# Optimization experiments

Measured on AMD Instinct MI355X. Metric: run time of the kernel, lower is better.

The kernel has to match this reference:

```python
import jax, jax.numpy as jnp
import numpy as np

B, T, SEG = 64, 16, 50          # batch, n segments, segment length (cap 50 in original)
E, D, H, F = 512, 512, 8, 2048  # dim_embeddings, dim_encoder, n_heads, dim_ff
DH = D // H
SCALE = float(1.0 / np.sqrt(DH))


def _ln(x, g, b):
    m = jnp.mean(x, -1, keepdims=True)
    v = jnp.var(x, -1, keepdims=True)
    return (x - m) * jax.lax.rsqrt(v + 1e-5) * g + b


def _mha(q_in, kv_in, Wq, Wk, Wv, Wo, kv_lens):
    b, sq, _ = q_in.shape
    sk = kv_in.shape[1]
    q = (q_in @ Wq).reshape(b, sq, H, DH)
    k = (kv_in @ Wk).reshape(b, sk, H, DH)
    v = (kv_in @ Wv).reshape(b, sk, H, DH)
    scores = jnp.einsum('bqhd,bkhd->bhqk', q, k) * SCALE
    mask = jnp.arange(sk)[None, :] < kv_lens[:, None]  # [b, sk] key-padding mask
    scores = jnp.where(mask[:, None, None, :], scores, -1e9)
    a = jax.nn.softmax(scores, axis=-1)
    o = jnp.einsum('bhqk,bkhd->bqhd', a, v).reshape(b, sq, D)
    return o @ Wo


def _ffn(x, W1, W2):
    return jax.nn.relu(x @ W1) @ W2


def _encoder(x, lens, p):
    # TransformerEncoder: project E->D, masked self-attn + FFN, post-LN residuals
    h = x @ p['eWin']
    h = _ln(h + _mha(h, h, p['eWq'], p['eWk'], p['eWv'], p['eWo'], lens), p['eG1'], p['eB1'])
    return _ln(h + _ffn(h, p['eF1'], p['eF2']), p['eG2'], p['eB2'])


def _connection(prev, curr, prev_lens, p):
    # Connection: curr cross-attends over prev (masked by prev_lens) + FFN
    h = _ln(curr + _mha(curr, prev, p['cWq'], p['cWk'], p['cWv'], p['cWo'], prev_lens), p['cG1'], p['cB1'])
    return _ln(h + _ffn(h, p['cF1'], p['cF2']), p['cG2'], p['cB2'])


def _forward(seqs, ends, p):
    first_lens = jnp.minimum(ends[:, 0], SEG)
    encoded = _encoder(seqs[:, :SEG], first_lens, p)  # [B, SEG, D]
    # regular segmentation: ends[b,t] = (t+1)*SEG, so every step uses a full segment
    segs = seqs.reshape(B, T, SEG, E).transpose(1, 0, 2, 3)[1:]        # [T-1, B, SEG, E]
    seg_lens = jnp.minimum(ends[:, 1:] - ends[:, :-1], SEG).T          # [T-1, B]
    prev_lens = jnp.full((B,), SEG, jnp.int32)

    def step(enc, xs):
        seg, lens = xs
        currs = _encoder(seg, lens, p)
        out = _connection(enc, currs, prev_lens, p)
        return out, None  # out[-SEG:] == out since seq_len = min(diff, 50) = SEG

    encoded, _ = jax.lax.scan(step, encoded, (segs, seg_lens))
    return encoded


def setup_inputs():
    key = jax.random.key(0)
    ks = jax.random.split(key, 16)
    g = lambda k, s: jax.random.normal(k, s, jnp.float32) * 0.02
    inp = {
        'seqs': jax.random.normal(ks[0], (B, T * SEG, E), jnp.float32),
        'ends': jnp.broadcast_to((jnp.arange(1, T + 1) * SEG).astype(jnp.int32), (B, T)),
        'eWin': g(ks[1], (E, D)),
        'eWq': g(ks[2], (D, D)), 'eWk': g(ks[3], (D, D)),
        'eWv': g(ks[4], (D, D)), 'eWo': g(ks[5], (D, D)),
        'eG1': jnp.ones(D), 'eB1': jnp.zeros(D),
        'eF1': g(ks[6], (D, F)), 'eF2': g(ks[7], (F, D)),
        'eG2': jnp.ones(D), 'eB2': jnp.zeros(D),
        'cWq': g(ks[8], (D, D)), 'cWk': g(ks[9], (D, D)),
        'cWv': g(ks[10], (D, D)), 'cWo': g(ks[11], (D, D)),
        'cG1': jnp.ones(D), 'cB1': jnp.zeros(D),
        'cF1': g(ks[12], (D, F)), 'cF2': g(ks[13], (F, D)),
        'cG2': jnp.ones(D), 'cB2': jnp.zeros(D),
    }
    return inp


def reference(seqs, ends, eWin, eWq, eWk, eWv, eWo, eG1, eB1, eF1, eF2, eG2, eB2,
              cWq, cWk, cWv, cWo, cG1, cB1, cF1, cF2, cG2, cB2):
    p = dict(eWin=eWin, eWq=eWq, eWk=eWk, eWv=eWv, eWo=eWo, eG1=eG1, eB1=eB1,
             eF1=eF1, eF2=eF2, eG2=eG2, eB2=eB2, cWq=cWq, cWk=cWk, cWv=cWv,
             cWo=cWo, cG1=cG1, cB1=cB1, cF1=cF1, cF2=cF2, cG2=cG2, cB2=cB2)
    return _forward(seqs, ends, p)
```

## Files before the change

kernel.cpp:

```cpp
#include <hip/hip_runtime.h>


#define NB   64
#define NT   16
#define SEGL 50
#define DMODEL 512
#define DFF  2048
#define NHEAD 8
#define DHEAD 64

typedef unsigned short ushort_t;
typedef __attribute__((ext_vector_type(8))) short bfrag;
typedef __attribute__((ext_vector_type(4))) float ffrag;

__device__ __forceinline__ ushort_t f2b(float x) {
    union { float f; unsigned u; } c; c.f = x;
    unsigned r = c.u + 0x7fffu + ((c.u >> 16) & 1u);
    return (ushort_t)(r >> 16);
}

#define GLOAD_LDS16(g, l) __builtin_amdgcn_global_load_lds( \
    (const __attribute__((address_space(1))) void*)(g),      \
    (__attribute__((address_space(3))) void*)(l), 16, 0, 0)

template<int BM, int BN, int WROWS, int WCOLS>
__global__ __launch_bounds__(256) void mfma_gemm(
    const ushort_t* __restrict__ A, int agrp, long long astride,
    const ushort_t* __restrict__ Bt, ushort_t* __restrict__ C,
    int M, int N, int K, int relu)
{
    constexpr int WM = BM / WROWS, WN = BN / WCOLS;
    constexpr int SM = WM / 16, SN = WN / 16;
    constexpr int NSUBA = BM / 16, NSUBB = BN / 16;
    constexpr int NSUB = NSUBA + NSUBB;
    constexpr int NINST = NSUB * 2;
    constexpr int IPW = NINST / 4;
    constexpr int BUFS = NSUB * 1024;
    constexpr int EST = WN + 8;
    constexpr int LDS_KLOOP = 2 * BUFS;
    constexpr int LDS_EPI   = 4 * WM * EST;
    constexpr int LDS_SZ = LDS_KLOOP > LDS_EPI ? LDS_KLOOP : LDS_EPI;
    __shared__ ushort_t lds[LDS_SZ];

    const int tid = threadIdx.x;
    const int wave = tid >> 6, lane = tid & 63;
    const int wrow = wave / WCOLS, wcol = wave % WCOLS;
    const int bm = blockIdx.y * BM, bn = blockIdx.x * BN;
    const int lm = lane & 15, lq = lane >> 4;

    ffrag acc[SM][SN];
#pragma unroll
    for (int i = 0; i < SM; ++i)
#pragma unroll
        for (int j = 0; j < SN; ++j) acc[i][j] = (ffrag){0.f, 0.f, 0.f, 0.f};

    const ushort_t* gptr[IPW];
    int loff[IPW];
#pragma unroll
    for (int e = 0; e < IPW; ++e) {
        int g = wave * IPW + e;
        int s = g >> 1, h = g & 1;
        if (s < NSUBA) {
            int m = bm + s * 16 + lm;
            gptr[e] = A + (long long)(m / agrp) * astride
                        + (long long)(m % agrp) * K + h * 32 + lq * 8;
        } else {
            int n = bn + (s - NSUBA) * 16 + lm;
            gptr[e] = Bt + (long long)n * K + h * 32 + lq * 8;
        }
        loff[e] = s * 1024 + h * 512;
    }

#pragma unroll
    for (int e = 0; e < IPW; ++e)
        GLOAD_LDS16(gptr[e], &lds[loff[e]]);

    const int nk = K >> 6;
    for (int kk = 0; kk < nk; ++kk) {
        __syncthreads();
        if (kk + 1 < nk) {
            const int koff = (kk + 1) << 6;
            const int nb = (kk + 1) & 1;
#pragma unroll
            for (int e = 0; e < IPW; ++e)
                GLOAD_LDS16(gptr[e] + koff, &lds[nb * BUFS + loff[e]]);
        }
        const ushort_t* lb = &lds[(kk & 1) * BUFS];
#pragma unroll
        for (int h = 0; h < 2; ++h) {
            bfrag af[SM], bfg[SN];
#pragma unroll
            for (int i = 0; i < SM; ++i)
                af[i] = *(const bfrag*)&lb[(wrow * SM + i) * 1024 + h * 512 + lane * 8];
#pragma unroll
            for (int j = 0; j < SN; ++j)
                bfg[j] = *(const bfrag*)&lb[(NSUBA + wcol * SN + j) * 1024 + h * 512 + lane * 8];
#pragma unroll
            for (int i = 0; i < SM; ++i)
#pragma unroll
                for (int j = 0; j < SN; ++j)
                    acc[i][j] = __builtin_amdgcn_mfma_f32_16x16x32_bf16(
                        af[i], bfg[j], acc[i][j], 0, 0, 0);
        }
    }

    __syncthreads();
    ushort_t* ep = &lds[wave * WM * EST];
#pragma unroll
    for (int i = 0; i < SM; ++i)
#pragma unroll
        for (int j = 0; j < SN; ++j)
#pragma unroll
            for (int r = 0; r < 4; ++r) {
                int row = i * 16 + lq * 4 + r;
                int col = j * 16 + lm;
                float v = acc[i][j][r];
                if (relu) v = fmaxf(v, 0.f);
                ep[row * EST + col] = f2b(v);
            }
    constexpr int CPR = WN / 8;
    constexpr int RPI = 64 / CPR;
    const int lrow = lane / CPR, lcol = (lane % CPR) * 8;
#pragma unroll
    for (int it = 0; it < WM / RPI; ++it) {
        int row = it * RPI + lrow;
        uint4 v = *(const uint4*)&ep[row * EST + lcol];
        long long grow = bm + wrow * WM + row;
        int gcol = bn + wcol * WN + lcol;
        *(uint4*)&C[grow * N + gcol] = v;
    }
}

__global__ __launch_bounds__(256) void wtrans_k(
    const float* __restrict__ W, ushort_t* __restrict__ Wt, int K, int N)
{
    __shared__ float t[32][33];
    const int bk = blockIdx.y * 32, bn = blockIdx.x * 32;
    const int tx = threadIdx.x & 31, ty = threadIdx.x >> 5;
    for (int i = ty; i < 32; i += 8)
        t[i][tx] = W[(long long)(bk + i) * N + bn + tx];
    __syncthreads();
    for (int i = ty; i < 32; i += 8)
        Wt[(long long)(bn + i) * K + bk + tx] = f2b(t[tx][i]);
}

__global__ __launch_bounds__(256) void cvt_k(
    const float* __restrict__ in, ushort_t* __restrict__ out, long long n)
{
    long long i = ((long long)blockIdx.x * 256 + threadIdx.x) * 8;
    if (i >= n) return;
    float4 a = *(const float4*)(in + i);
    float4 b = *(const float4*)(in + i + 4);
    ushort_t o[8] = {f2b(a.x), f2b(a.y), f2b(a.z), f2b(a.w),
                     f2b(b.x), f2b(b.y), f2b(b.z), f2b(b.w)};
    *(uint4*)(out + i) = *(const uint4*)o;
}

__global__ __launch_bounds__(256) void attn_mfma_k(
    const ushort_t* __restrict__ Q, long long qns, long long qrs,
    const ushort_t* __restrict__ K, const ushort_t* __restrict__ V,
    long long kns, long long kvrs,
    ushort_t* __restrict__ O,
    const int* __restrict__ lens, int G, int t0)
{
    __shared__ ushort_t qs[64][72];
    __shared__ ushort_t ks[64][72];
    __shared__ ushort_t vt[64][72];
    const int n = blockIdx.x >> 3, h = blockIdx.x & 7;
    const int tid = threadIdx.x;
    const int wave = tid >> 6, lane = tid & 63;
    const int lm = lane & 15, lq = lane >> 4;
    int len = SEGL;
    if (lens) {
        int b = n / G, t = t0 + (n % G);
        len = lens[b * NT + t];
        if (len > SEGL) len = SEGL;
    }
    {
        uint4 z = {0, 0, 0, 0};
        uint4* vz = (uint4*)&vt[0][0];
        for (int i = tid; i < 64 * 72 / 8; i += 256) vz[i] = z;
    }
    __syncthreads();
    for (int idx = tid; idx < SEGL * 8; idx += 256) {
        int s = idx >> 3, d8 = (idx & 7) << 3;
        const ushort_t* qp = Q + (long long)n * qns + (long long)s * qrs + h * DHEAD + d8;
        const ushort_t* kp = K + (long long)n * kns + (long long)s * kvrs + h * DHEAD + d8;
        const ushort_t* vp = V + (long long)n * kns + (long long)s * kvrs + h * DHEAD + d8;
        *(uint4*)&qs[s][d8] = *(const uint4*)qp;
        *(uint4*)&ks[s][d8] = *(const uint4*)kp;
        uint4 v4 = *(const uint4*)vp;
        const ushort_t* vv = (const ushort_t*)&v4;
#pragma unroll
        for (int u = 0; u < 8; ++u) vt[d8 + u][s] = vv[u];
    }
    __syncthreads();

    ffrag sc[4];
#pragma unroll
    for (int nt = 0; nt < 4; ++nt) sc[nt] = (ffrag){0.f, 0.f, 0.f, 0.f};
#pragma unroll
    for (int kt = 0; kt < 2; ++kt) {
        bfrag a = *(const bfrag*)&qs[wave * 16 + lm][kt * 32 + lq * 8];
#pragma unroll
        for (int nt = 0; nt < 4; ++nt) {
            bfrag b = *(const bfrag*)&ks[nt * 16 + lm][kt * 32 + lq * 8];
            sc[nt] = __builtin_amdgcn_mfma_f32_16x16x32_bf16(a, b, sc[nt], 0, 0, 0);
        }
    }
    __syncthreads();

#pragma unroll
    for (int r = 0; r < 4; ++r) {
        float x[4];
        float mx = -1e30f;
#pragma unroll
        for (int nt = 0; nt < 4; ++nt) {
            int col = nt * 16 + lm;
            x[nt] = (col < len) ? sc[nt][r] * 0.125f : -1e9f;
            mx = fmaxf(mx, x[nt]);
        }
        for (int off = 8; off; off >>= 1) mx = fmaxf(mx, __shfl_xor(mx, off));
        float e[4], se = 0.f;
#pragma unroll
        for (int nt = 0; nt < 4; ++nt) { e[nt] = __expf(x[nt] - mx); se += e[nt]; }
        for (int off = 8; off; off >>= 1) se += __shfl_xor(se, off);
        float inv = 1.f / se;
        int row = wave * 16 + lq * 4 + r;
#pragma unroll
        for (int nt = 0; nt < 4; ++nt)
            qs[row][nt * 16 + lm] = f2b(e[nt] * inv);
    }
    __syncthreads();

    ffrag oc[4];
#pragma unroll
    for (int dt = 0; dt < 4; ++dt) oc[dt] = (ffrag){0.f, 0.f, 0.f, 0.f};
#pragma unroll
    for (int kt = 0; kt < 2; ++kt) {
        bfrag a = *(const bfrag*)&qs[wave * 16 + lm][kt * 32 + lq * 8];
#pragma unroll
        for (int dt = 0; dt < 4; ++dt) {
            bfrag b = *(const bfrag*)&vt[dt * 16 + lm][kt * 32 + lq * 8];
            oc[dt] = __builtin_amdgcn_mfma_f32_16x16x32_bf16(a, b, oc[dt], 0, 0, 0);
        }
    }
#pragma unroll
    for (int r = 0; r < 4; ++r) {
        int i = wave * 16 + lq * 4 + r;
        if (i < SEGL) {
            ushort_t* op = O + (long long)(n * SEGL + i) * DMODEL + h * DHEAD + lm;
#pragma unroll
            for (int dt = 0; dt < 4; ++dt)
                op[dt * 16] = f2b(oc[dt][r]);
        }
    }
}

template<bool OUTF32>
__global__ __launch_bounds__(256) void add_ln_k(
    const ushort_t* __restrict__ A, int agrp, long long astride,
    const ushort_t* __restrict__ Bv,
    const float* __restrict__ gamma, const float* __restrict__ beta,
    void* __restrict__ O, int ogrp, long long ostride, int M)
{
    const int wave = threadIdx.x >> 6, lane = threadIdx.x & 63;
    const int r = blockIdx.x * 4 + wave;
    if (r >= M) return;
    const ushort_t* a = A + (long long)(r / agrp) * astride + (long long)(r % agrp) * DMODEL;
    const ushort_t* b = Bv + (long long)r * DMODEL;
    float x[8];
    {
        uint4 a4 = *(const uint4*)(a + lane * 8);
        uint4 b4 = *(const uint4*)(b + lane * 8);
        const unsigned* aa = (const unsigned*)&a4;
        const unsigned* bb = (const unsigned*)&b4;
#pragma unroll
        for (int c = 0; c < 4; ++c) {
            union { unsigned u; float f; } alo, ahi, blo, bhi;
            alo.u = aa[c] << 16; ahi.u = aa[c] & 0xffff0000u;
            blo.u = bb[c] << 16; bhi.u = bb[c] & 0xffff0000u;
            x[2 * c]     = alo.f + blo.f;
            x[2 * c + 1] = ahi.f + bhi.f;
        }
    }
    float s = 0.f, s2 = 0.f;
#pragma unroll
    for (int i = 0; i < 8; ++i) { s += x[i]; s2 = fmaf(x[i], x[i], s2); }
    for (int off = 32; off; off >>= 1) {
        s += __shfl_xor(s, off);
        s2 += __shfl_xor(s2, off);
    }
    const float mean = s * (1.f / DMODEL);
    const float var = s2 * (1.f / DMODEL) - mean * mean;
    const float inv = rsqrtf(var + 1e-5f);
    float4 g0 = *(const float4*)(gamma + lane * 8);
    float4 g1 = *(const float4*)(gamma + lane * 8 + 4);
    float4 be0 = *(const float4*)(beta + lane * 8);
    float4 be1 = *(const float4*)(beta + lane * 8 + 4);
    float y[8];
    y[0] = (x[0] - mean) * inv * g0.x + be0.x;
    y[1] = (x[1] - mean) * inv * g0.y + be0.y;
    y[2] = (x[2] - mean) * inv * g0.z + be0.z;
    y[3] = (x[3] - mean) * inv * g0.w + be0.w;
    y[4] = (x[4] - mean) * inv * g1.x + be1.x;
    y[5] = (x[5] - mean) * inv * g1.y + be1.y;
    y[6] = (x[6] - mean) * inv * g1.z + be1.z;
    y[7] = (x[7] - mean) * inv * g1.w + be1.w;
    if (OUTF32) {
        float* o = (float*)O + (long long)(r / ogrp) * ostride + (long long)(r % ogrp) * DMODEL;
        *(float4*)(o + lane * 8) = *(float4*)&y[0];
        *(float4*)(o + lane * 8 + 4) = *(float4*)&y[4];
    } else {
        ushort_t* o = (ushort_t*)O + (long long)(r / ogrp) * ostride + (long long)(r % ogrp) * DMODEL;
        ushort_t ob[8];
#pragma unroll
        for (int i = 0; i < 8; ++i) ob[i] = f2b(y[i]);
        *(uint4*)(o + lane * 8) = *(const uint4*)ob;
    }
}

__global__ void lens_k(const int* __restrict__ ends, int* __restrict__ lens)
{
    int i = blockIdx.x * 256 + threadIdx.x;
    if (i >= NB * NT) return;
    int t = i & (NT - 1);
    int prev = t ? ends[i - 1] : 0;
    int l = ends[i] - prev;
    if (l > SEGL) l = SEGL;
    lens[i] = l;
}

extern "C" void kernel_launch(void* const* d_in, const int* in_sizes, int n_in,
                              void* d_out, int out_size, void* d_ws, size_t ws_size,
                              hipStream_t stream)
{
    const float* seqs = (const float*)d_in[0];
    const int*   ends = (const int*)d_in[1];
    const float* eG1 = (const float*)d_in[7],  *eB1 = (const float*)d_in[8];
    const float* eG2 = (const float*)d_in[11], *eB2 = (const float*)d_in[12];
    const float* cG1 = (const float*)d_in[17], *cB1 = (const float*)d_in[18];
    const float* cG2 = (const float*)d_in[21], *cB2 = (const float*)d_in[22];
    float* out = (float*)d_out;

    const int G = (ws_size >= (size_t)470000000) ? 8 : 4;
    const long long CH = 1638400LL * G;

    ushort_t* ws = (ushort_t*)d_ws;
    const long long SEQROW = (long long)NT * SEGL * DMODEL;
    ushort_t* SEQB = ws;
    ushort_t* WT   = SEQB + 26214400LL;
    ushort_t* ENC  = WT   + 6553600LL;
    ushort_t* BUF0 = ENC  + 26214400LL;
    ushort_t* QKV  = BUF0 + CH;
    ushort_t* BUF4 = QKV  + 3 * CH;
    ushort_t* BUF1 = BUF4 + CH;
    ushort_t* BUF2 = BUF1 + CH;
    ushort_t* MID  = BUF2 + CH;
    ushort_t* OUTB = MID  + 4 * CH;
    ushort_t* QALL = OUTB + 1638400LL;
    int*      lens = (int*)(QALL + 24576000LL);

    const ushort_t* eWinT = WT + 0;
    const ushort_t* WQKVe = WT + 262144;
    const ushort_t* eWoT  = WT + 1048576;
    const ushort_t* eF1T  = WT + 1310720;
    const ushort_t* eF2T  = WT + 2359296;
    const ushort_t* cWqT  = WT + 3407872;
    const ushort_t* cKV   = WT + 3670016;
    const ushort_t* cWoT  = WT + 4194304;
    const ushort_t* cF1T  = WT + 4456448;
    const ushort_t* cF2T  = WT + 5505024;

    struct WMap { int src; long long dst; int K, N; };
    const WMap wm[13] = {
        {2,  0,       512, 512},
        {3,  262144,  512, 512},
        {4,  524288,  512, 512},
        {5,  786432,  512, 512},
        {6,  1048576, 512, 512},
        {9,  1310720, 512, 2048},
        {10, 2359296, 2048, 512},
        {13, 3407872, 512, 512},
        {14, 3670016, 512, 512},
        {15, 3932160, 512, 512},
        {16, 4194304, 512, 512},
        {19, 4456448, 512, 2048},
        {20, 5505024, 2048, 512},
    };

    cvt_k<<<12800, 256, 0, stream>>>(seqs, SEQB, 26214400LL);
    for (int w = 0; w < 13; ++w) {
        dim3 g(wm[w].N / 32, wm[w].K / 32);
        wtrans_k<<<g, 256, 0, stream>>>((const float*)d_in[wm[w].src],
                                        WT + wm[w].dst, wm[w].K, wm[w].N);
    }
    lens_k<<<4, 256, 0, stream>>>(ends, lens);

    auto gemmL = [&](const ushort_t* A, int agrp, long long astr, const ushort_t* Bt,
                     ushort_t* C, int M, int N, int K, int relu) {
        dim3 g(N / 128, M / 128);
        mfma_gemm<128, 128, 2, 2><<<g, 256, 0, stream>>>(A, agrp, astr, Bt, C, M, N, K, relu);
    };
    auto gemmS = [&](const ushort_t* A, int agrp, long long astr, const ushort_t* Bt,
                     ushort_t* C, int M, int N, int K, int relu) {
        dim3 g(N / 128, M / 64);
        mfma_gemm<64, 128, 2, 2><<<g, 256, 0, stream>>>(A, agrp, astr, Bt, C, M, N, K, relu);
    };

    const int Mc = NB * G * SEGL;
    for (int c = 0; c < NT / G; ++c) {
        const int t0 = c * G;
        const ushort_t* Abase = SEQB + (long long)t0 * SEGL * DMODEL;
        ushort_t* ENCc = ENC + (long long)t0 * SEGL * DMODEL;
        gemmL(Abase, G * SEGL, SEQROW, eWinT, BUF0, Mc, 512, 512, 0);
        gemmL(BUF0, Mc, 0, WQKVe, QKV, Mc, 1536, 512, 0);
        attn_mfma_k<<<NB * G * NHEAD, 256, 0, stream>>>(
            QKV, 50LL * 1536, 1536, QKV + 512, QKV + 1024, 50LL * 1536, 1536,
            BUF4, lens, G, t0);
        gemmL(BUF4, Mc, 0, eWoT, BUF1, Mc, 512, 512, 0);
        add_ln_k<false><<<Mc / 4, 256, 0, stream>>>(BUF0, Mc, 0, BUF1, eG1, eB1,
                                                    BUF2, Mc, 0, Mc);
        gemmL(BUF2, Mc, 0, eF1T, MID, Mc, 2048, 512, 1);
        gemmL(MID, Mc, 0, eF2T, BUF1, Mc, 512, 2048, 0);
        add_ln_k<false><<<Mc / 4, 256, 0, stream>>>(BUF2, Mc, 0, BUF1, eG2, eB2,
                                                    ENCc, G * SEGL, SEQROW, Mc);
    }

    gemmL(ENC + 25600, 750, SEQROW, cWqT, QALL, 48000, 512, 512, 0);

    const int Ms = NB * SEGL;
    for (int t = 1; t < NT; ++t) {
        const ushort_t* currA = ENC + (long long)t * SEGL * DMODEL;
        const ushort_t* prevA; int pg; long long ps;
        if (t == 1) { prevA = ENC;  pg = SEGL; ps = SEQROW; }
        else        { prevA = OUTB; pg = Ms;   ps = 0; }
        gemmS(prevA, pg, ps, cKV, QKV, Ms, 1024, 512, 0);
        attn_mfma_k<<<NB * NHEAD, 256, 0, stream>>>(
            QALL + (long long)(t - 1) * 25600, 750LL * 512, 512,
            QKV, QKV + 512, 50LL * 1024, 1024,
            BUF4, nullptr, 1, 0);
        gemmS(BUF4, Ms, 0, cWoT, BUF0, Ms, 512, 512, 0);
        add_ln_k<false><<<Ms / 4, 256, 0, stream>>>(currA, SEGL, SEQROW, BUF0, cG1, cB1,
                                                    BUF2, Ms, 0, Ms);
        gemmS(BUF2, Ms, 0, cF1T, MID, Ms, 2048, 512, 1);
        gemmS(MID, Ms, 0, cF2T, BUF0, Ms, 512, 2048, 0);
        if (t == NT - 1)
            add_ln_k<true><<<Ms / 4, 256, 0, stream>>>(BUF2, Ms, 0, BUF0, cG2, cB2,
                                                       out, Ms, 0, Ms);
        else
            add_ln_k<false><<<Ms / 4, 256, 0, stream>>>(BUF2, Ms, 0, BUF0, cG2, cB2,
                                                        OUTB, Ms, 0, Ms);
    }
}
```

Before: 2.845 ms.

## Use register-only wave-tiled GEMM for small sequential connection-step matmuls

Adds a new GEMM kernel in which each wave loads A and B fragments straight from global memory into registers, double-buffered over K, with no LDS staging, using 64x64 block tiles. It replaces the 64x128 LDS-tiled GEMM for the four per-step matmuls in the serial connection loop (M=3200). The aim is to launch more blocks so the small GEMMs fill more CUs, and to drop LDS barriers. In exchange, operands are no longer reused across waves through shared memory, so global and L2 traffic goes up.

```diff
diff --git a/kernel.cpp b/kernel.cpp
--- a/kernel.cpp
+++ b/kernel.cpp
@@ -128,6 +128,96 @@
         long long grow = bm + wrow * WM + row;
         int gcol = bn + wcol * WN + lcol;
         *(uint4*)&C[grow * N + gcol] = v;
+    }
+}
+
+template<int SM, int SN>
+__global__ __launch_bounds__(256) void wave_gemm(
+    const ushort_t* __restrict__ A, int agrp, long long astride,
+    const ushort_t* __restrict__ Bt, ushort_t* __restrict__ C,
+    int M, int N, int K, int relu)
+{
+    constexpr int WM = SM * 16, WN = SN * 16;
+    constexpr int EST = WN + 8;
+    __shared__ ushort_t ep[4][WM][EST];
+    const int tid = threadIdx.x;
+    const int wave = tid >> 6, lane = tid & 63;
+    const int wrow = wave >> 1, wcol = wave & 1;
+    const int lm = lane & 15, lq = lane >> 4;
+    const int bm = blockIdx.y * (2 * WM) + wrow * WM;
+    const int bn = blockIdx.x * (2 * WN) + wcol * WN;
+
+    const ushort_t* ap[SM];
+    const ushort_t* bp[SN];
+#pragma unroll
+    for (int i = 0; i < SM; ++i) {
+        int m = bm + i * 16 + lm;
+        ap[i] = A + (long long)(m / agrp) * astride + (long long)(m % agrp) * K + lq * 8;
+    }
+#pragma unroll
+    for (int j = 0; j < SN; ++j) {
+        int n = bn + j * 16 + lm;
+        bp[j] = Bt + (long long)n * K + lq * 8;
+    }
+
+    ffrag acc[SM][SN];
+#pragma unroll
+    for (int i = 0; i < SM; ++i)
+#pragma unroll
+        for (int j = 0; j < SN; ++j) acc[i][j] = (ffrag){0.f, 0.f, 0.f, 0.f};
+
+    bfrag a0[SM], b0[SN], a1[SM], b1[SN];
+#pragma unroll
+    for (int i = 0; i < SM; ++i) a0[i] = *(const bfrag*)(ap[i]);
+#pragma unroll
+    for (int j = 0; j < SN; ++j) b0[j] = *(const bfrag*)(bp[j]);
+
+    const int nk = K >> 5;
+    for (int kk = 0; kk < nk; kk += 2) {
+        const int k1 = (kk + 1) << 5;
+#pragma unroll
+        for (int i = 0; i < SM; ++i) a1[i] = *(const bfrag*)(ap[i] + k1);
+#pragma unroll
+        for (int j = 0; j < SN; ++j) b1[j] = *(const bfrag*)(bp[j] + k1);
+#pragma unroll
+        for (int i = 0; i < SM; ++i)
+#pragma unroll
+            for (int j = 0; j < SN; ++j)
+                acc[i][j] = __builtin_amdgcn_mfma_f32_16x16x32_bf16(
+                    a0[i], b0[j], acc[i][j], 0, 0, 0);
+        if (kk + 2 < nk) {
+            const int k2 = (kk + 2) << 5;
+#pragma unroll
+            for (int i = 0; i < SM; ++i) a0[i] = *(const bfrag*)(ap[i] + k2);
+#pragma unroll
+            for (int j = 0; j < SN; ++j) b0[j] = *(const bfrag*)(bp[j] + k2);
+        }
+#pragma unroll
+        for (int i = 0; i < SM; ++i)
+#pragma unroll
+            for (int j = 0; j < SN; ++j)
+                acc[i][j] = __builtin_amdgcn_mfma_f32_16x16x32_bf16(
+                    a1[i], b1[j], acc[i][j], 0, 0, 0);
+    }
+
+#pragma unroll
+    for (int i = 0; i < SM; ++i)
+#pragma unroll
+        for (int j = 0; j < SN; ++j)
+#pragma unroll
+            for (int r = 0; r < 4; ++r) {
+                float v = acc[i][j][r];
+                if (relu) v = fmaxf(v, 0.f);
+                ep[wave][i * 16 + lq * 4 + r][j * 16 + lm] = f2b(v);
+            }
+    constexpr int CPR = WN / 8;
+    constexpr int RPI = 64 / CPR;
+    const int lrow = lane / CPR, lcol = (lane % CPR) * 8;
+#pragma unroll
+    for (int it = 0; it < WM / RPI; ++it) {
+        int row = it * RPI + lrow;
+        uint4 v = *(const uint4*)&ep[wave][row][lcol];
+        *(uint4*)&C[(long long)(bm + row) * N + bn + lcol] = v;
     }
 }
 
@@ -402,10 +492,10 @@
         dim3 g(N / 128, M / 128);
         mfma_gemm<128, 128, 2, 2><<<g, 256, 0, stream>>>(A, agrp, astr, Bt, C, M, N, K, relu);
     };
-    auto gemmS = [&](const ushort_t* A, int agrp, long long astr, const ushort_t* Bt,
+    auto gemmW = [&](const ushort_t* A, int agrp, long long astr, const ushort_t* Bt,
                      ushort_t* C, int M, int N, int K, int relu) {
-        dim3 g(N / 128, M / 64);
-        mfma_gemm<64, 128, 2, 2><<<g, 256, 0, stream>>>(A, agrp, astr, Bt, C, M, N, K, relu);
+        dim3 g(N / 64, M / 64);
+        wave_gemm<2, 2><<<g, 256, 0, stream>>>(A, agrp, astr, Bt, C, M, N, K, relu);
     };
 
     const int Mc = NB * G * SEGL;
@@ -435,16 +525,16 @@
         const ushort_t* prevA; int pg; long long ps;
         if (t == 1) { prevA = ENC;  pg = SEGL; ps = SEQROW; }
         else        { prevA = OUTB; pg = Ms;   ps = 0; }
-        gemmS(prevA, pg, ps, cKV, QKV, Ms, 1024, 512, 0);
+        gemmW(prevA, pg, ps, cKV, QKV, Ms, 1024, 512, 0);
         attn_mfma_k<<<NB * NHEAD, 256, 0, stream>>>(
             QALL + (long long)(t - 1) * 25600, 750LL * 512, 512,
             QKV, QKV + 512, 50LL * 1024, 1024,
             BUF4, nullptr, 1, 0);
-        gemmS(BUF4, Ms, 0, cWoT, BUF0, Ms, 512, 512, 0);
+        gemmW(BUF4, Ms, 0, cWoT, BUF0, Ms, 512, 512, 0);
         add_ln_k<false><<<Ms / 4, 256, 0, stream>>>(currA, SEGL, SEQROW, BUF0, cG1, cB1,
                                                     BUF2, Ms, 0, Ms);
-        gemmS(BUF2, Ms, 0, cF1T, MID, Ms, 2048, 512, 1);
-        gemmS(MID, Ms, 0, cF2T, BUF0, Ms, 512, 2048, 0);
+        gemmW(BUF2, Ms, 0, cF1T, MID, Ms, 2048, 512, 1);
+        gemmW(MID, Ms, 0, cF2T, BUF0, Ms, 512, 2048, 0);
         if (t == NT - 1)
             add_ln_k<true><<<Ms / 4, 256, 0, stream>>>(BUF2, Ms, 0, BUF0, cG2, cB2,
                                                        out, Ms, 0, Ms);
```

Measured after the change: 3.907 ms. 1.37x slower.

## Fuse cross-attention K/V projection into attention kernel and shrink small GEMM tiles

Applied to the files above, without the earlier changes.

Adds a cross_attn_k kernel in which each (batch, head) block computes its own K and V head slices from the previous segment's output using MFMA. It then runs masked softmax attention in the same kernel, so the separate K/V projection GEMM and its QKV buffer round trip are removed from each sequential step. The small-M GEMM tile also drops from 64x128 to 64x64 to give the serial per-step GEMMs more blocks. In exchange, weight fragments are read straight from global memory with no LDS reuse across blocks, and each block redoes projection work that the old GEMM shared.

```diff
diff --git a/kernel.cpp b/kernel.cpp
--- a/kernel.cpp
+++ b/kernel.cpp
@@ -218,6 +218,143 @@
         for (int nt = 0; nt < 4; ++nt) {
             int col = nt * 16 + lm;
             x[nt] = (col < len) ? sc[nt][r] * 0.125f : -1e9f;
+            mx = fmaxf(mx, x[nt]);
+        }
+        for (int off = 8; off; off >>= 1) mx = fmaxf(mx, __shfl_xor(mx, off));
+        float e[4], se = 0.f;
+#pragma unroll
+        for (int nt = 0; nt < 4; ++nt) { e[nt] = __expf(x[nt] - mx); se += e[nt]; }
+        for (int off = 8; off; off >>= 1) se += __shfl_xor(se, off);
+        float inv = 1.f / se;
+        int row = wave * 16 + lq * 4 + r;
+#pragma unroll
+        for (int nt = 0; nt < 4; ++nt)
+            qs[row][nt * 16 + lm] = f2b(e[nt] * inv);
+    }
+    __syncthreads();
+
+    ffrag oc[4];
+#pragma unroll
+    for (int dt = 0; dt < 4; ++dt) oc[dt] = (ffrag){0.f, 0.f, 0.f, 0.f};
+#pragma unroll
+    for (int kt = 0; kt < 2; ++kt) {
+        bfrag a = *(const bfrag*)&qs[wave * 16 + lm][kt * 32 + lq * 8];
+#pragma unroll
+        for (int dt = 0; dt < 4; ++dt) {
+            bfrag b = *(const bfrag*)&vt[dt * 16 + lm][kt * 32 + lq * 8];
+            oc[dt] = __builtin_amdgcn_mfma_f32_16x16x32_bf16(a, b, oc[dt], 0, 0, 0);
+        }
+    }
+#pragma unroll
+    for (int r = 0; r < 4; ++r) {
+        int i = wave * 16 + lq * 4 + r;
+        if (i < SEGL) {
+            ushort_t* op = O + (long long)(n * SEGL + i) * DMODEL + h * DHEAD + lm;
+#pragma unroll
+            for (int dt = 0; dt < 4; ++dt)
+                op[dt * 16] = f2b(oc[dt][r]);
+        }
+    }
+}
+
+__global__ __launch_bounds__(256) void cross_attn_k(
+    const ushort_t* __restrict__ Qp, long long qns, long long qrs,
+    const ushort_t* __restrict__ Prev, int pgrp, long long pstride,
+    const ushort_t* __restrict__ Wkv,
+    ushort_t* __restrict__ O)
+{
+    __shared__ ushort_t xp[64 * 264];
+    __shared__ ushort_t qs[64][72];
+    const int n = blockIdx.x >> 3, h = blockIdx.x & 7;
+    const int tid = threadIdx.x;
+    const int wave = tid >> 6, lane = tid & 63;
+    const int lm = lane & 15, lq = lane >> 4;
+
+    for (int idx = tid; idx < SEGL * 8; idx += 256) {
+        int s = idx >> 3, d8 = (idx & 7) << 3;
+        *(uint4*)&qs[s][d8] =
+            *(const uint4*)(Qp + (long long)n * qns + (long long)s * qrs + h * DHEAD + d8);
+    }
+
+    const ushort_t* wbase = Wkv +
+        (long long)((wave >> 1) * 512 + h * 64 + (wave & 1) * 32) * 512;
+    ffrag kv[4][2];
+#pragma unroll
+    for (int i = 0; i < 4; ++i)
+#pragma unroll
+        for (int j = 0; j < 2; ++j) kv[i][j] = (ffrag){0.f, 0.f, 0.f, 0.f};
+
+#pragma unroll
+    for (int half = 0; half < 2; ++half) {
+        __syncthreads();
+        for (int idx = tid; idx < 64 * 33; idx += 256) {
+            int s = idx / 33, c8 = (idx % 33) * 8;
+            uint4 v = {0, 0, 0, 0};
+            if (s < SEGL && c8 < 256) {
+                long long r = (long long)n * SEGL + s;
+                v = *(const uint4*)(Prev + (r / pgrp) * pstride
+                                    + (r % pgrp) * DMODEL + half * 256 + c8);
+            }
+            *(uint4*)&xp[s * 264 + c8] = v;
+        }
+        __syncthreads();
+#pragma unroll
+        for (int k8 = 0; k8 < 8; ++k8) {
+            const int kg = half * 256 + k8 * 32;
+            bfrag bf[2], af[4];
+#pragma unroll
+            for (int j = 0; j < 2; ++j)
+                bf[j] = *(const bfrag*)(wbase + (long long)(j * 16 + lm) * 512 + kg + lq * 8);
+#pragma unroll
+            for (int i = 0; i < 4; ++i)
+                af[i] = *(const bfrag*)&xp[(i * 16 + lm) * 264 + k8 * 32 + lq * 8];
+#pragma unroll
+            for (int i = 0; i < 4; ++i)
+#pragma unroll
+                for (int j = 0; j < 2; ++j)
+                    kv[i][j] = __builtin_amdgcn_mfma_f32_16x16x32_bf16(
+                        af[i], bf[j], kv[i][j], 0, 0, 0);
+        }
+    }
+    __syncthreads();
+    ushort_t (*ks)[72] = (ushort_t(*)[72])&xp[0];
+    ushort_t (*vt)[72] = (ushort_t(*)[72])&xp[64 * 72];
+#pragma unroll
+    for (int i = 0; i < 4; ++i)
+#pragma unroll
+        for (int j = 0; j < 2; ++j)
+#pragma unroll
+            for (int r = 0; r < 4; ++r) {
+                int rowk = i * 16 + lq * 4 + r;
+                int d = (wave & 1) * 32 + j * 16 + lm;
+                ushort_t val = f2b(kv[i][j][r]);
+                if (wave < 2) ks[rowk][d] = val;
+                else          vt[d][rowk] = val;
+            }
+    __syncthreads();
+
+    ffrag sc[4];
+#pragma unroll
+    for (int nt = 0; nt < 4; ++nt) sc[nt] = (ffrag){0.f, 0.f, 0.f, 0.f};
+#pragma unroll
+    for (int kt = 0; kt < 2; ++kt) {
+        bfrag a = *(const bfrag*)&qs[wave * 16 + lm][kt * 32 + lq * 8];
+#pragma unroll
+        for (int nt = 0; nt < 4; ++nt) {
+            bfrag b = *(const bfrag*)&ks[nt * 16 + lm][kt * 32 + lq * 8];
+            sc[nt] = __builtin_amdgcn_mfma_f32_16x16x32_bf16(a, b, sc[nt], 0, 0, 0);
+        }
+    }
+    __syncthreads();
+
+#pragma unroll
+    for (int r = 0; r < 4; ++r) {
+        float x[4];
+        float mx = -1e30f;
+#pragma unroll
+        for (int nt = 0; nt < 4; ++nt) {
+            int col = nt * 16 + lm;
+            x[nt] = (col < SEGL) ? sc[nt][r] * 0.125f : -1e9f;
             mx = fmaxf(mx, x[nt]);
         }
         for (int off = 8; off; off >>= 1) mx = fmaxf(mx, __shfl_xor(mx, off));
@@ -404,8 +541,8 @@
     };
     auto gemmS = [&](const ushort_t* A, int agrp, long long astr, const ushort_t* Bt,
                      ushort_t* C, int M, int N, int K, int relu) {
-        dim3 g(N / 128, M / 64);
-        mfma_gemm<64, 128, 2, 2><<<g, 256, 0, stream>>>(A, agrp, astr, Bt, C, M, N, K, relu);
+        dim3 g(N / 64, M / 64);
+        mfma_gemm<64, 64, 2, 2><<<g, 256, 0, stream>>>(A, agrp, astr, Bt, C, M, N, K, relu);
     };
 
     const int Mc = NB * G * SEGL;
@@ -435,11 +572,9 @@
         const ushort_t* prevA; int pg; long long ps;
         if (t == 1) { prevA = ENC;  pg = SEGL; ps = SEQROW; }
         else        { prevA = OUTB; pg = Ms;   ps = 0; }
-        gemmS(prevA, pg, ps, cKV, QKV, Ms, 1024, 512, 0);
-        attn_mfma_k<<<NB * NHEAD, 256, 0, stream>>>(
+        cross_attn_k<<<NB * NHEAD, 256, 0, stream>>>(
             QALL + (long long)(t - 1) * 25600, 750LL * 512, 512,
-            QKV, QKV + 512, 50LL * 1024, 1024,
-            BUF4, nullptr, 1, 0);
+            prevA, pg, ps, cKV, BUF4);
         gemmS(BUF4, Ms, 0, cWoT, BUF0, Ms, 512, 512, 0);
         add_ln_k<false><<<Ms / 4, 256, 0, stream>>>(currA, SEGL, SEQROW, BUF0, cG1, cB1,
                                                     BUF2, Ms, 0, Ms);
```

Result: faster. 2.767 ms (-2.8%).
